# Performance work log

Measured on AMD Instinct MI355X. Metric: run time of the kernel, lower is better.

The kernel has to match this reference:

```python
import jax, jax.numpy as jnp
import numpy as np

NUM_TYPES = 4
SPLINE_GRID = 5   # grid centers on [0, 1]
SPLINE_SPAN = 3   # number of overlapping basis functions -> degree P = 2
CHANNELS = 64
E = 500_000
P = SPLINE_SPAN - 1
NUM_BASIS = (SPLINE_GRID - 1) + P  # intervals + degree = 6


def _knots_np():
    # uniform knots extended by P beyond each end of [0, 1]
    h = 1.0 / (SPLINE_GRID - 1)
    return ((np.arange(NUM_BASIS + P + 1) - P) * h).astype(np.float32)


def bspline_basis(x):
    """Uniform B-spline basis of degree P via Cox-de Boor. x: [E] in [0,1] -> [E, NUM_BASIS]."""
    t = jnp.asarray(_knots_np(), dtype=x.dtype)
    xe = jnp.clip(x, 0.0, 1.0 - 1e-6)[:, None]
    # degree-0: indicator of the knot interval  [E, NUM_BASIS + P]
    B = ((xe >= t[None, :-1]) & (xe < t[None, 1:])).astype(x.dtype)
    for k in range(1, P + 1):
        left = (xe - t[None, : -(k + 1)]) / (t[k:-1] - t[: -(k + 1)])[None, :] * B[:, :-1]
        right = (t[None, k + 1 :] - xe) / (t[k + 1 :] - t[1:-k])[None, :] * B[:, 1:]
        B = left + right
    return B  # [E, NUM_BASIS]


def setup_inputs() -> dict:
    key = jax.random.key(0)
    k1, k2, k3 = jax.random.split(key, 3)
    x = jax.random.uniform(k1, (E,), dtype=jnp.float32)                 # normalized edge lengths in [0,1]
    edge_types = jax.random.randint(k2, (2, E), 0, NUM_TYPES)           # (center, neighbor) atom types
    coeffs = jax.random.normal(
        k3, (NUM_TYPES * NUM_TYPES, NUM_BASIS, CHANNELS), dtype=jnp.float32
    )  # per-edge-type spline coefficients
    return {"x": x, "edge_types": edge_types, "coeffs": coeffs}


def reference(x, edge_types, coeffs):
    # edge class = center_type * num_types + neighbor_type
    cls = edge_types[0] * NUM_TYPES + edge_types[1]      # [E]
    basis = bspline_basis(x)                             # [E, NUM_BASIS]
    # gather per-edge coefficients and reduce over the local spline support
    return jnp.einsum("eb,ebc->ec", basis, coeffs[cls])  # [E, CHANNELS]
```

## Files before the change

kernel.cpp:

```cpp
#include <hip/hip_runtime.h>

constexpr int NUM_TYPES    = 4;
constexpr int NUM_BASIS    = 6;
constexpr int CHANNELS     = 64;
constexpr int COEFF_FLOATS = NUM_TYPES * NUM_TYPES * NUM_BASIS * CHANNELS;

typedef float f4 __attribute__((ext_vector_type(4)));

__global__ __launch_bounds__(256)
void TwoBodySplineScalarEmbed_kernel(const float* __restrict__ x,
                                     const int*   __restrict__ edge_types,
                                     const float* __restrict__ coeffs,
                                     float*       __restrict__ out,
                                     int E)
{
    __shared__ float sc[COEFF_FLOATS];
    #pragma unroll
    for (int i = 0; i < COEFF_FLOATS / 4 / 256; ++i) {
        int idx = threadIdx.x + i * 256;
        reinterpret_cast<f4*>(sc)[idx] = reinterpret_cast<const f4*>(coeffs)[idx];
    }
    __syncthreads();

    const int laneC  = threadIdx.x & 15;
    const int grp    = threadIdx.x >> 4;
    const int c0     = laneC * 4;
    const int stride = gridDim.x << 4;

    for (int e = (blockIdx.x << 4) + grp; e < E; e += stride)
    {
        float xj = fminf(fmaxf(x[e], 0.0f), 1.0f - 1e-6f);
        float s  = xj * 4.0f;
        int   i0 = (int)s;  i0 = i0 > 3 ? 3 : i0;
        float u  = s - (float)i0;
        float omu = 1.0f - u;
        float w0 = 0.5f * omu * omu;
        float w1 = u * omu + 0.5f;
        float w2 = 0.5f * u * u;

        int row = (edge_types[e] * NUM_TYPES + edge_types[E + e]) * NUM_BASIS + i0;
        const float* base = &sc[row * CHANNELS + c0];
        f4 r0 = *reinterpret_cast<const f4*>(base);
        f4 r1 = *reinterpret_cast<const f4*>(base + CHANNELS);
        f4 r2 = *reinterpret_cast<const f4*>(base + 2 * CHANNELS);

        f4 o = w0 * r0 + w1 * r1 + w2 * r2;
        *reinterpret_cast<f4*>(out + (size_t)e * CHANNELS + c0) = o;
    }
}

extern "C" void kernel_launch(void* const* d_in, const int* in_sizes, int n_in,
                              void* d_out, int out_size, void* d_ws, size_t ws_size,
                              hipStream_t stream)
{
    const float* x          = (const float*)d_in[0];
    const int*   edge_types = (const int*)d_in[1];
    const float* coeffs     = (const float*)d_in[2];
    float*       out        = (float*)d_out;

    const int E = in_sizes[0];

    int grid = (E + 15) / 16;
    if (grid > 1536) grid = 1536;

    TwoBodySplineScalarEmbed_kernel<<<grid, 256, 0, stream>>>(
        x, edge_types, coeffs, out, E);
}
```

Before: 27.74 us.

## Batch-stage per-edge x and class rows into shared memory before compute

Each block now loads x and edge-type pairs for up to 21 strided edge batches cooperatively into shared memory, one element per thread, then runs the spline evaluation from LDS. Previously each 16-lane group redundantly loaded the same x and edge_types values. This cuts redundant global loads and front-loads them so they can overlap. It adds barriers per outer iteration and a staging phase, and the kernel remains bound by output stores.

```diff
diff --git a/kernel.cpp b/kernel.cpp
--- a/kernel.cpp
+++ b/kernel.cpp
@@ -4,6 +4,8 @@
 constexpr int NUM_BASIS    = 6;
 constexpr int CHANNELS     = 64;
 constexpr int COEFF_FLOATS = NUM_TYPES * NUM_TYPES * NUM_BASIS * CHANNELS;
+constexpr int KMAX  = 21;
+constexpr int SLOTS = 16 * KMAX;
 
 typedef float f4 __attribute__((ext_vector_type(4)));
 
@@ -14,38 +16,57 @@
                                      float*       __restrict__ out,
                                      int E)
 {
-    __shared__ float sc[COEFF_FLOATS];
+    __shared__ float          sc[COEFF_FLOATS];
+    __shared__ float          sx[SLOTS];
+    __shared__ unsigned short srow[SLOTS];
+
     #pragma unroll
     for (int i = 0; i < COEFF_FLOATS / 4 / 256; ++i) {
         int idx = threadIdx.x + i * 256;
         reinterpret_cast<f4*>(sc)[idx] = reinterpret_cast<const f4*>(coeffs)[idx];
     }
-    __syncthreads();
 
     const int laneC  = threadIdx.x & 15;
     const int grp    = threadIdx.x >> 4;
     const int c0     = laneC * 4;
     const int stride = gridDim.x << 4;
+    const int t      = threadIdx.x;
 
-    for (int e = (blockIdx.x << 4) + grp; e < E; e += stride)
+    for (int base = blockIdx.x << 4; base < E; base += stride * KMAX)
     {
-        float xj = fminf(fmaxf(x[e], 0.0f), 1.0f - 1e-6f);
-        float s  = xj * 4.0f;
-        int   i0 = (int)s;  i0 = i0 > 3 ? 3 : i0;
-        float u  = s - (float)i0;
-        float omu = 1.0f - u;
-        float w0 = 0.5f * omu * omu;
-        float w1 = u * omu + 0.5f;
-        float w2 = 0.5f * u * u;
+        for (int s = t; s < SLOTS; s += 256) {
+            int e = base + (s & 15) + (s >> 4) * stride;
+            if (e < E) {
+                sx[s]   = x[e];
+                srow[s] = (unsigned short)((edge_types[e] * NUM_TYPES +
+                                            edge_types[E + e]) * NUM_BASIS);
+            }
+        }
+        __syncthreads();
 
-        int row = (edge_types[e] * NUM_TYPES + edge_types[E + e]) * NUM_BASIS + i0;
-        const float* base = &sc[row * CHANNELS + c0];
-        f4 r0 = *reinterpret_cast<const f4*>(base);
-        f4 r1 = *reinterpret_cast<const f4*>(base + CHANNELS);
-        f4 r2 = *reinterpret_cast<const f4*>(base + 2 * CHANNELS);
+        for (int k = 0; k < KMAX; ++k) {
+            int e = base + grp + k * stride;
+            if (e >= E) break;
+            int s = (k << 4) + grp;
 
-        f4 o = w0 * r0 + w1 * r1 + w2 * r2;
-        *reinterpret_cast<f4*>(out + (size_t)e * CHANNELS + c0) = o;
+            float xj = fminf(fmaxf(sx[s], 0.0f), 1.0f - 1e-6f);
+            float sx4 = xj * 4.0f;
+            int   i0  = (int)sx4;  i0 = i0 > 3 ? 3 : i0;
+            float u   = sx4 - (float)i0;
+            float omu = 1.0f - u;
+            float w0 = 0.5f * omu * omu;
+            float w1 = u * omu + 0.5f;
+            float w2 = 0.5f * u * u;
+
+            const float* bp = &sc[(srow[s] + i0) * CHANNELS + c0];
+            f4 r0 = *reinterpret_cast<const f4*>(bp);
+            f4 r1 = *reinterpret_cast<const f4*>(bp + CHANNELS);
+            f4 r2 = *reinterpret_cast<const f4*>(bp + 2 * CHANNELS);
+
+            f4 o = w0 * r0 + w1 * r1 + w2 * r2;
+            *reinterpret_cast<f4*>(out + (size_t)e * CHANNELS + c0) = o;
+        }
+        __syncthreads();
     }
 }
 
```

Result: faster. 27.13 us (median of 2 runs) (-2.2%).
